# Kernel tuning notes

Hardware: AMD Instinct MI355X
Metric: run time of the kernel (lower is better)

## Reference

```python
import jax, jax.numpy as jnp
import numpy as np

B, C, H, W = 2, 64, 48, 48
NH = 8
EPS = 1e-5


def conv2d(x, w, b=None, pad=0):
    out = jax.lax.conv_general_dilated(x, w, (1, 1), [(pad, pad), (pad, pad)],
                                       dimension_numbers=('NCHW', 'OIHW', 'NCHW'))
    return out if b is None else out + b[None, :, None, None]


def bn2d(x, g, b, m, v):
    # eval-mode BatchNorm2d with running stats
    return (x - m[None, :, None, None]) * (g / jnp.sqrt(v + EPS))[None, :, None, None] + b[None, :, None, None]


def ln(x, g, b):
    mu = x.mean(-1, keepdims=True)
    var = ((x - mu) ** 2).mean(-1, keepdims=True)
    return (x - mu) / jnp.sqrt(var + EPS) * g + b


def _forward(x, y, pconv_w, pconv_b, bnd_g, bnd_b, bnd_m, bnd_v,
             lnx_g, lnx_b, lny_g, lny_b, lnz_g, lnz_b,
             k_w, k_b, qv_w, qv_b, proj_w, proj_b,
             c2w1, c2b1, c2bn1_g, c2bn1_b, c2bn1_m, c2bn1_v,
             c2w2, c2b2, c2bn2_g, c2bn2_b, c2bn2_m, c2bn2_v,
             bn2_g, bn2_b, bn2_m, bn2_v,
             f1w, fbn1_g, fbn1_b, fbn1_m, fbn1_v,
             f2w, fbn2_g, fbn2_b, fbn2_m, fbn2_v,
             f3w, f3b):
    Bq, Cq, Hq, Wq = x.shape
    N = Hq * Wq
    hd = Cq // NH
    scale = hd ** -0.5
    xy = conv2d(jnp.concatenate([x, y], 1), pconv_w, pconv_b, pad=0)
    xb = bn2d(x, bnd_g, bnd_b, bnd_m, bnd_v)
    yb = bn2d(y, bnd_g, bnd_b, bnd_m, bnd_v)
    xyb = bn2d(xy, bnd_g, bnd_b, bnd_m, bnd_v)
    sc1 = xb.reshape(Bq, Cq, N).transpose(0, 2, 1)  # [B,N,C]
    sd1 = yb.reshape(Bq, Cq, N).transpose(0, 2, 1)
    xl = ln(sc1, lnx_g, lnx_b)
    yl = ln(sd1, lny_g, lny_b)
    zl = ln(xyb.reshape(Bq, Cq, N).transpose(0, 2, 1), lnz_g, lnz_b)

    def qv_heads(t):
        qv = (t @ qv_w.T + qv_b).reshape(Bq, N, 2, NH, hd)
        return qv[:, :, 0].transpose(0, 2, 1, 3), qv[:, :, 1].transpose(0, 2, 1, 3)

    x_q, x_v = qv_heads(xl)
    y_q, y_v = qv_heads(yl)
    k = (zl @ k_w.T + k_b).reshape(Bq, N, NH, hd).transpose(0, 2, 1, 3)  # [B,H,N,hd]
    attn1 = jnp.einsum('bhnd,bhmd->bhnm', x_q, k) * scale
    attn2 = jnp.einsum('bhnd,bhmd->bhnm', y_q, k) * scale
    attn = jax.nn.softmax(attn1 * attn2, axis=-1)  # product of two score maps
    xo = jnp.einsum('bhnm,bhmd->bhnd', attn, x_v).transpose(0, 2, 1, 3).reshape(Bq, N, Cq) @ proj_w.T + proj_b
    yo = jnp.einsum('bhnm,bhmd->bhnd', attn, y_v).transpose(0, 2, 1, 3).reshape(Bq, N, Cq) @ proj_w.T + proj_b
    xo = (xo + sc1).transpose(0, 2, 1).reshape(Bq, Cq, Hq, Wq)
    yo = (yo + sd1).transpose(0, 2, 1).reshape(Bq, Cq, Hq, Wq)

    def conv2_block(t):  # shared-weight conv2 applied to both branches
        h = jax.nn.relu(bn2d(conv2d(t, c2w1, c2b1, pad=1), c2bn1_g, c2bn1_b, c2bn1_m, c2bn1_v))
        return jax.nn.relu(bn2d(conv2d(h, c2w2, c2b2, pad=1), c2bn2_g, c2bn2_b, c2bn2_m, c2bn2_v))

    xo = conv2_block(xo) + xo
    yo = conv2_block(yo) + yo
    cat = jnp.concatenate([xo + yo, xo * yo], 1)  # [B,2C,H,W]
    f = bn2d(cat, bn2_g, bn2_b, bn2_m, bn2_v)
    f = jax.nn.relu(bn2d(conv2d(f, f1w, None, pad=1), fbn1_g, fbn1_b, fbn1_m, fbn1_v))
    f = jax.nn.relu(bn2d(conv2d(f, f2w, None, pad=1), fbn2_g, fbn2_b, fbn2_m, fbn2_v))
    f = conv2d(f, f3w, f3b, pad=0)
    return cat + f


def setup_inputs() -> dict:
    ks = iter(jax.random.split(jax.random.key(0), 64))

    def nrm(shape, s=0.05):
        return jax.random.normal(next(ks), shape, jnp.float32) * s

    def bn_params(c):
        return (1.0 + nrm((c,)), nrm((c,)), nrm((c,)),
                jax.random.uniform(next(ks), (c,), jnp.float32, 0.5, 1.5))

    d = {}
    d['x'] = jax.random.normal(next(ks), (B, C, H, W), jnp.float32)
    d['y'] = jax.random.normal(next(ks), (B, C, H, W), jnp.float32)
    d['pconv_w'] = nrm((C, 2 * C, 1, 1)); d['pconv_b'] = nrm((C,))
    d['bnd_g'], d['bnd_b'], d['bnd_m'], d['bnd_v'] = bn_params(C)
    d['lnx_g'] = 1.0 + nrm((C,)); d['lnx_b'] = nrm((C,))
    d['lny_g'] = 1.0 + nrm((C,)); d['lny_b'] = nrm((C,))
    d['lnz_g'] = 1.0 + nrm((C,)); d['lnz_b'] = nrm((C,))
    d['k_w'] = nrm((C, C)); d['k_b'] = nrm((C,))
    d['qv_w'] = nrm((2 * C, C)); d['qv_b'] = nrm((2 * C,))
    d['proj_w'] = nrm((C, C)); d['proj_b'] = nrm((C,))
    d['c2w1'] = nrm((C, C, 3, 3)); d['c2b1'] = nrm((C,))
    d['c2bn1_g'], d['c2bn1_b'], d['c2bn1_m'], d['c2bn1_v'] = bn_params(C)
    d['c2w2'] = nrm((C, C, 3, 3)); d['c2b2'] = nrm((C,))
    d['c2bn2_g'], d['c2bn2_b'], d['c2bn2_m'], d['c2bn2_v'] = bn_params(C)
    d['bn2_g'], d['bn2_b'], d['bn2_m'], d['bn2_v'] = bn_params(2 * C)
    d['f1w'] = nrm((2 * C, 2 * C, 3, 3))
    d['fbn1_g'], d['fbn1_b'], d['fbn1_m'], d['fbn1_v'] = bn_params(2 * C)
    d['f2w'] = nrm((2 * C, 2 * C, 3, 3))
    d['fbn2_g'], d['fbn2_b'], d['fbn2_m'], d['fbn2_v'] = bn_params(2 * C)
    d['f3w'] = nrm((2 * C, 2 * C, 1, 1)); d['f3b'] = nrm((2 * C,))
    return d


def reference(x, y, pconv_w, pconv_b, bnd_g, bnd_b, bnd_m, bnd_v,
              lnx_g, lnx_b, lny_g, lny_b, lnz_g, lnz_b,
              k_w, k_b, qv_w, qv_b, proj_w, proj_b,
              c2w1, c2b1, c2bn1_g, c2bn1_b, c2bn1_m, c2bn1_v,
              c2w2, c2b2, c2bn2_g, c2bn2_b, c2bn2_m, c2bn2_v,
              bn2_g, bn2_b, bn2_m, bn2_v,
              f1w, fbn1_g, fbn1_b, fbn1_m, fbn1_v,
              f2w, fbn2_g, fbn2_b, fbn2_m, fbn2_v,
              f3w, f3b):
    return _forward(x, y, pconv_w, pconv_b, bnd_g, bnd_b, bnd_m, bnd_v,
                    lnx_g, lnx_b, lny_g, lny_b, lnz_g, lnz_b,
                    k_w, k_b, qv_w, qv_b, proj_w, proj_b,
                    c2w1, c2b1, c2bn1_g, c2bn1_b, c2bn1_m, c2bn1_v,
                    c2w2, c2b2, c2bn2_g, c2bn2_b, c2bn2_m, c2bn2_v,
                    bn2_g, bn2_b, bn2_m, bn2_v,
                    f1w, fbn1_g, fbn1_b, fbn1_m, fbn1_v,
                    f2w, fbn2_g, fbn2_b, fbn2_m, fbn2_v,
                    f3w, f3b)
```

## Files before the change

kernel.cpp:

```cpp
#include <hip/hip_runtime.h>
#include <hip/hip_bf16.h>

#define B_   2
#define C_   64
#define H_   48
#define W_   48
#define N_   (H_*W_)
#define NH_  8
#define HD_  8
#define EPS_ 1e-5f
#define S2_  0.125f
#define LOG2E_ 1.44269504f
#define FS_  (S2_ * LOG2E_)
#define S_   ((size_t)B_ * C_ * N_)
#define CN_  ((size_t)C_ * N_)
#define XTSZ_ ((size_t)(N_ + 2 * W_) * 128)
#define XTSC_ ((size_t)(N_ + 2 * W_) * 64)

typedef unsigned short u16;
typedef __attribute__((ext_vector_type(8))) short short8v;
typedef __attribute__((ext_vector_type(4))) float f32x4;
union F8 { uint4 u4; short8v s; unsigned int w[4]; };

__device__ __forceinline__ float wsum64(float v) {
#pragma unroll
  for (int o = 32; o > 0; o >>= 1) v += __shfl_xor(v, o, 64);
  return v;
}

__device__ __forceinline__ float ln_val(float t, float g, float b) {
  float mu  = wsum64(t) * (1.0f / 64.0f);
  float d   = t - mu;
  float var = wsum64(d * d) * (1.0f / 64.0f);
  return d * rsqrtf(var + EPS_) * g + b;
}

__device__ __forceinline__ u16 f2bf(float x) {
  union { float f; unsigned int u; } a; a.f = x;
  unsigned int r = a.u + 0x7fffu + ((a.u >> 16) & 1u);
  return (u16)(r >> 16);
}

__global__ __launch_bounds__(1024) void k_pre(
    const float* __restrict__ x, const float* __restrict__ y,
    const float* __restrict__ pw, const float* __restrict__ pb,
    const float* g, const float* bb, const float* m, const float* v,
    const float* lnxg, const float* lnxb,
    const float* lnyg, const float* lnyb,
    const float* lnzg, const float* lnzb,
    float* __restrict__ xl, float* __restrict__ yl, float* __restrict__ zl) {
  __shared__ float4 pwT[32][64];
  __shared__ float xs[16][64], ys[16][64];
  int w = threadIdx.x >> 6, c = threadIdx.x & 63;
  for (int idx = threadIdx.x; idx < 2048; idx += 1024) {
    int cc = idx & 63, i4 = idx >> 6;
    pwT[i4][cc] = *(const float4*)(pw + (size_t)cc * 2 * C_ + i4 * 4);
  }
  int row = blockIdx.x * 16 + w;
  int b = row / N_, n = row % N_;
  float xv = x[(size_t)(b * C_ + c) * N_ + n];
  float yv = y[(size_t)(b * C_ + c) * N_ + n];
  xs[w][c] = xv; ys[w][c] = yv;
  __syncthreads();
  const float4* xw = (const float4*)xs[w];
  const float4* yw = (const float4*)ys[w];
  float acc = pb[c];
#pragma unroll
  for (int t = 0; t < 16; ++t) {
    float4 a = xw[t], wv = pwT[t][c];
    acc += a.x * wv.x + a.y * wv.y + a.z * wv.z + a.w * wv.w;
  }
#pragma unroll
  for (int t = 0; t < 16; ++t) {
    float4 a = yw[t], wv = pwT[16 + t][c];
    acc += a.x * wv.x + a.y * wv.y + a.z * wv.z + a.w * wv.w;
  }
  float s  = g[c] * rsqrtf(v[c] + EPS_);
  float sh = bb[c] - m[c] * s;
  float tx = xv * s + sh;
  xl[(size_t)row * C_ + c] = ln_val(tx, lnxg[c], lnxb[c]);
  float ty = yv * s + sh;
  yl[(size_t)row * C_ + c] = ln_val(ty, lnyg[c], lnyb[c]);
  float tz = acc * s + sh;
  zl[(size_t)row * C_ + c] = ln_val(tz, lnzg[c], lnzb[c]);
}

__global__ __launch_bounds__(64) void k_qvk(
    const float* __restrict__ xl, const float* __restrict__ yl,
    const float* __restrict__ zl,
    const float* __restrict__ qvw, const float* __restrict__ qvb,
    const float* __restrict__ kw, const float* __restrict__ kb,
    u16* __restrict__ qxb, u16* __restrict__ qyb,
    u16* __restrict__ kbf, u16* __restrict__ vt) {
  int l = threadIdx.x;
  int part = blockIdx.y >> 2;
  int j0 = (blockIdx.y & 3) * 16;
  int row = blockIdx.x * 64 + l;
  int b = row / N_, n = row % N_;
  const float* inp = (part < 2) ? xl : (part < 4) ? yl : zl;
  float4 in[16];
  const float4* ir = (const float4*)(inp + (size_t)row * C_);
#pragma unroll
  for (int t = 0; t < 16; ++t) in[t] = ir[t];

  const float* wb   = (part == 4) ? kw : qvw;
  const float* bias = (part == 4) ? kb : qvb;
  int joff = (part == 1 || part == 3) ? 64 : 0;

  if (part == 1 || part == 3) {
    int vbase = (part == 1) ? 0 : 8;
#pragma unroll
    for (int jj = 0; jj < 16; ++jj) {
      int j = j0 + jj;
      const float4* wr = (const float4*)(wb + (size_t)(joff + j) * C_);
      float acc = bias[joff + j];
#pragma unroll
      for (int t = 0; t < 16; ++t) {
        float4 a = in[t], wv = wr[t];
        acc += a.x * wv.x + a.y * wv.y + a.z * wv.z + a.w * wv.w;
      }
      int h = j >> 3, d = j & 7;
      vt[((size_t)((b * NH_ + h) * 16 + vbase + d)) * N_ + n] = f2bf(acc);
    }
  } else {
    u16* dst = (part == 0) ? qxb : (part == 2) ? qyb : kbf;
#pragma unroll
    for (int gg = 0; gg < 2; ++gg) {
      int h = (j0 >> 3) + gg;
      union { uint4 u4; u16 s[8]; } pk;
#pragma unroll
      for (int d = 0; d < 8; ++d) {
        int j = h * 8 + d;
        const float4* wr = (const float4*)(wb + (size_t)(joff + j) * C_);
        float acc = bias[joff + j];
#pragma unroll
        for (int t = 0; t < 16; ++t) {
          float4 a = in[t], wv = wr[t];
          acc += a.x * wv.x + a.y * wv.y + a.z * wv.z + a.w * wv.w;
        }
        if (part == 0) acc *= FS_;
        pk.s[d] = f2bf(acc);
      }
      *(uint4*)(dst + ((size_t)(b * NH_ + h) * N_ + n) * 8) = pk.u4;
    }
  }
}

__global__ __launch_bounds__(128, 5) void k_attn8(
    const u16* __restrict__ qx, const u16* __restrict__ qy,
    const u16* __restrict__ kk, const u16* __restrict__ vt,
    float* __restrict__ outx, float* __restrict__ outy) {
  __shared__ float sAcc[2][4][64];
  __shared__ float sL[2][16];
  int qt = blockIdx.x, bh = blockIdx.y;
  int tid = threadIdx.x;
  int lane = tid & 63;
  int wave = tid >> 6;
  int l15 = lane & 15;
  int q0 = qt * 16;

  F8 qxf, qyf;
  size_t qoff = ((size_t)bh * N_ + q0 + l15) * 8;
  qxf.u4 = *(const uint4*)(qx + qoff);
  qyf.u4 = *(const uint4*)(qy + qoff);
  if (lane >= 16) {
    qxf.u4 = make_uint4(0u, 0u, 0u, 0u);
    qyf.u4 = make_uint4(0u, 0u, 0u, 0u);
  }

  int key0 = wave * (N_ / 2);
  const uint4* kp = (const uint4*)(kk + (size_t)bh * N_ * 8) + key0 + l15;
  const uint4* vp = (const uint4*)(vt + ((size_t)bh * 16 + l15) * N_ + key0)
                    + (lane >> 4);
  int addr0 = (((lane >> 4) & 1) * 32 + l15) * 4;
  int addr1 = addr0 + 64;
  int thi = lane >> 5;

  f32x4 acc = {0.f, 0.f, 0.f, 0.f};
  const f32x4 z4 = {0.f, 0.f, 0.f, 0.f};
  float lsum = 0.f;

  F8 ka, kb2, vf;
  ka.u4 = kp[0]; kb2.u4 = kp[16]; vf.u4 = *vp;
  for (int c = 0; c < 36; ++c) {
    F8 kaC = ka, kbC = kb2, vfC = vf;
    kp += 32; vp += 4;
    ka.u4 = kp[0]; kb2.u4 = kp[16]; vf.u4 = *vp;

    f32x4 s1a = __builtin_amdgcn_mfma_f32_16x16x32_bf16(kaC.s, qxf.s, z4, 0, 0, 0);
    f32x4 s2a = __builtin_amdgcn_mfma_f32_16x16x32_bf16(kaC.s, qyf.s, z4, 0, 0, 0);
    f32x4 s1b = __builtin_amdgcn_mfma_f32_16x16x32_bf16(kbC.s, qxf.s, z4, 0, 0, 0);
    f32x4 s2b = __builtin_amdgcn_mfma_f32_16x16x32_bf16(kbC.s, qyf.s, z4, 0, 0, 0);

    float p00 = exp2f(s1a[0] * s2a[0]), p01 = exp2f(s1a[1] * s2a[1]);
    float p02 = exp2f(s1a[2] * s2a[2]), p03 = exp2f(s1a[3] * s2a[3]);
    float p10 = exp2f(s1b[0] * s2b[0]), p11 = exp2f(s1b[1] * s2b[1]);
    float p12 = exp2f(s1b[2] * s2b[2]), p13 = exp2f(s1b[3] * s2b[3]);
    lsum += ((p00 + p01) + (p02 + p03)) + ((p10 + p11) + (p12 + p13));

    unsigned int pk00, pk10, pk01, pk11;
    asm("v_cvt_pk_bf16_f32 %0, %1, %2" : "=v"(pk00) : "v"(p00), "v"(p01));
    asm("v_cvt_pk_bf16_f32 %0, %1, %2" : "=v"(pk10) : "v"(p02), "v"(p03));
    asm("v_cvt_pk_bf16_f32 %0, %1, %2" : "=v"(pk01) : "v"(p10), "v"(p11));
    asm("v_cvt_pk_bf16_f32 %0, %1, %2" : "=v"(pk11) : "v"(p12), "v"(p13));

    int b00 = __builtin_amdgcn_ds_bpermute(addr0, (int)pk00);
    int b01 = __builtin_amdgcn_ds_bpermute(addr0, (int)pk01);
    int b10 = __builtin_amdgcn_ds_bpermute(addr0, (int)pk10);
    int b11 = __builtin_amdgcn_ds_bpermute(addr0, (int)pk11);
    int c00 = __builtin_amdgcn_ds_bpermute(addr1, (int)pk00);
    int c01 = __builtin_amdgcn_ds_bpermute(addr1, (int)pk01);
    int c10 = __builtin_amdgcn_ds_bpermute(addr1, (int)pk10);
    int c11 = __builtin_amdgcn_ds_bpermute(addr1, (int)pk11);

    F8 pf;
    pf.w[0] = (unsigned int)(thi ? b01 : b00);
    pf.w[1] = (unsigned int)(thi ? b11 : b10);
    pf.w[2] = (unsigned int)(thi ? c01 : c00);
    pf.w[3] = (unsigned int)(thi ? c11 : c10);
    acc = __builtin_amdgcn_mfma_f32_16x16x32_bf16(pf.s, vfC.s, acc, 0, 0, 0);
  }

  lsum += __shfl_xor(lsum, 16, 64);
  lsum += __shfl_xor(lsum, 32, 64);
  if (lane < 16) sL[wave][lane] = lsum;
#pragma unroll
  for (int r = 0; r < 4; ++r) sAcc[wave][r][lane] = acc[r];
  __syncthreads();
  if (wave == 0) {
    float Linv = 1.f / (sL[0][l15] + sL[1][l15]);
    int b = bh >> 3, h = bh & 7;
    int d = l15 & 7;
    float* ob = (l15 < 8) ? outx : outy;
    size_t cbase = (size_t)b * N_ * C_ + (size_t)h * 8 + d;
#pragma unroll
    for (int r = 0; r < 4; ++r) {
      int qrow = 4 * (lane >> 4) + r;
      float li = __shfl(Linv, qrow, 64);
      float a = sAcc[0][r][lane] + sAcc[1][r][lane];
      ob[cbase + (size_t)(q0 + qrow) * C_] = a * li;
    }
  }
}

__global__ __launch_bounds__(64) void k_proj4(
    const float* __restrict__ attbase,
    const float* __restrict__ x, const float* __restrict__ y,
    const float* bg, const float* bb2, const float* bm, const float* bv,
    const float* __restrict__ pw, const float* __restrict__ pbias,
    float* __restrict__ outbase, u16* __restrict__ xt0) {
  __shared__ float attT[64][66];
  int tid = threadIdx.x;
  int p0 = blockIdx.x * 64;
  int c0 = blockIdx.y * 2;
  int z = blockIdx.z;
  int branch = z >> 1, b = z & 1;
  const float* att = attbase + branch * S_ + (size_t)b * N_ * C_;
  for (int r = 0; r < 64; ++r)
    attT[tid][r] = att[(size_t)(p0 + r) * C_ + tid];
  __syncthreads();
  int p = p0 + tid;
  const float* w0 = pw + (size_t)c0 * C_;
  const float* w1 = w0 + C_;
  float a0 = pbias[c0], a1 = pbias[c0 + 1];
#pragma unroll 8
  for (int c = 0; c < C_; ++c) {
    float av = attT[c][tid];
    a0 += av * w0[c];
    a1 += av * w1[c];
  }
  float s0  = bg[c0] * rsqrtf(bv[c0] + EPS_);
  float sh0 = bb2[c0] - bm[c0] * s0;
  float s1  = bg[c0+1] * rsqrtf(bv[c0+1] + EPS_);
  float sh1 = bb2[c0+1] - bm[c0+1] * s1;
  const float* xin = branch ? y : x;
  float r0 = xin[((size_t)b * C_ + c0) * N_ + p];
  float r1 = xin[((size_t)b * C_ + c0 + 1) * N_ + p];
  float v0 = a0 + r0 * s0 + sh0;
  float v1 = a1 + r1 * s1 + sh1;
  size_t o = (size_t)z * CN_ + (size_t)c0 * N_ + p;
  outbase[o]      = v0;
  outbase[o + N_] = v1;
  unsigned int pv = ((unsigned int)f2bf(v1) << 16) | (unsigned int)f2bf(v0);
  *(unsigned int*)(xt0 + (size_t)z * XTSC_ + (size_t)(W_ + p) * 64 + c0) = pv;
}

__global__ void k_catbn(const float* __restrict__ o2,
                        const float* __restrict__ g, const float* __restrict__ b2,
                        const float* __restrict__ m, const float* __restrict__ v,
                        float* __restrict__ cat, u16* __restrict__ xt1) {
  int t = blockIdx.x * 256 + threadIdx.x;
  int p4 = t * 4;
  int n  = p4 % N_;
  int c2 = (p4 / N_) % (2 * C_);
  int b  = p4 / (2 * C_ * N_);
  int c  = c2 & 63;
  float4 X = *(const float4*)(o2 + (size_t)b * CN_ + (size_t)c * N_ + n);
  float4 Y = *(const float4*)(o2 + (size_t)(2 + b) * CN_ + (size_t)c * N_ + n);
  float4 val;
  if (c2 < C_) val = make_float4(X.x + Y.x, X.y + Y.y, X.z + Y.z, X.w + Y.w);
  else         val = make_float4(X.x * Y.x, X.y * Y.y, X.z * Y.z, X.w * Y.w);
  size_t co = ((size_t)b * 2 * C_ + c2) * N_ + n;
  *(float4*)(cat + co) = val;
  float s  = g[c2] * rsqrtf(v[c2] + EPS_);
  float sh = b2[c2] - m[c2] * s;
  u16* xb = xt1 + (size_t)b * XTSZ_ + (size_t)(W_ + n) * 128 + c2;
  xb[0]   = f2bf(val.x * s + sh);
  xb[128] = f2bf(val.y * s + sh);
  xb[256] = f2bf(val.z * s + sh);
  xb[384] = f2bf(val.w * s + sh);
}

__global__ void k_zg(u16* __restrict__ b0, u16* __restrict__ b1,
                     int nimg, int cinc) {
  int gsz = W_ * cinc / 2;
  int pbt = nimg * 2 * gsz;
  int idx = blockIdx.x * 256 + threadIdx.x;
  if (idx >= 2 * pbt) return;
  u16* base = (idx < pbt) ? b0 : b1;
  int r = idx % pbt;
  int img = r / (2 * gsz);
  int r2 = r % (2 * gsz);
  int hi = r2 / gsz, o = r2 % gsz;
  size_t xts = (size_t)(N_ + 2 * W_) * cinc;
  ((unsigned int*)(base + (size_t)img * xts
                   + (hi ? (size_t)(W_ + N_) * cinc : 0)))[o] = 0u;
}

__global__ void k_wcvt(const float* __restrict__ w1,
                       const float* __restrict__ w2,
                       const float* __restrict__ cw1,
                       const float* __restrict__ cw2,
                       u16* __restrict__ wb) {
  int idx = blockIdx.x * 256 + threadIdx.x;
  if (idx >= 368640) return;
  if (idx < 294912) {
    int layer = idx / 147456, rem = idx - layer * 147456;
    int t = rem / 16384, r2 = rem - t * 16384;
    int co = r2 >> 7, ci = r2 & 127;
    wb[idx] = f2bf((layer ? w2 : w1)[(size_t)co * 1152 + ci * 9 + t]);
  } else {
    int k = idx - 294912;
    int layer = k / 36864, rem = k - layer * 36864;
    int t = rem / 4096, r2 = rem - t * 4096;
    int co = r2 >> 6, ci = r2 & 63;
    wb[idx] = f2bf((layer ? cw2 : cw1)[(size_t)co * 576 + ci * 9 + t]);
  }
}

template<int MODE>
__global__ __launch_bounds__(64) void k_fmma(
    const u16* __restrict__ xt, const u16* __restrict__ wb,
    const float* __restrict__ cbias,
    const float* g, const float* b2, const float* m, const float* v,
    const float* __restrict__ resid,
    u16* __restrict__ xto, float* __restrict__ fo) {
  constexpr int CIN  = (MODE >= 2) ? 64 : 128;
  constexpr int NCB  = CIN / 32;
  constexpr int COUT = (MODE >= 2) ? 64 : 128;
  constexpr int TS   = CIN * COUT;
  constexpr size_t XTS = (size_t)(N_ + 2 * W_) * CIN;
  constexpr size_t XTSO = (size_t)(N_ + 2 * W_) * COUT;
  int l = threadIdx.x;
  int c = l & 15, gg = l >> 4;
  int px0 = blockIdx.x * 16;
  int ct0 = blockIdx.y * 16;
  int b = blockIdx.z;
  int x0 = px0 % W_;
  bool mL = (x0 == 0) && (c == 0);
  bool mR = (x0 == 32) && (c == 15);
  const u16* xb = xt + (size_t)b * XTS + (size_t)W_ * CIN;
  const u16* aw = wb + (size_t)(ct0 + c) * CIN + gg * 8;

  f32x4 acc = {0.f, 0.f, 0.f, 0.f};
#pragma unroll
  for (int cb = 0; cb < NCB; ++cb) {
#pragma unroll
    for (int t = 0; t < 9; ++t) {
      const int dx = t % 3 - 1, dy = t / 3 - 1;
      F8 af, bf;
      af.u4 = *(const uint4*)(aw + t * TS + cb * 32);
      int px = px0 + c + dx + dy * W_;
      px = max(px, -W_);
      bf.u4 = *(const uint4*)(xb + (ptrdiff_t)px * CIN + cb * 32 + gg * 8);
      bool msk = (dx < 0 && mL) || (dx > 0 && mR);
      if (msk) bf.u4 = make_uint4(0u, 0u, 0u, 0u);
      acc = __builtin_amdgcn_mfma_f32_16x16x32_bf16(af.s, bf.s, acc, 0, 0, 0);
    }
  }
  int px = px0 + c;
  if (MODE == 0 || MODE == 2) {
    union { ushort4 u; u16 s[4]; } pk;
#pragma unroll
    for (int r = 0; r < 4; ++r) {
      int cout = ct0 + 4 * gg + r;
      float a = acc[r] + (MODE == 2 ? cbias[cout] : 0.f);
      float s = g[cout] * rsqrtf(v[cout] + EPS_);
      float sh = b2[cout] - m[cout] * s;
      pk.s[r] = f2bf(fmaxf(a * s + sh, 0.f));
    }
    *(ushort4*)(xto + (size_t)b * XTSO + (size_t)(W_ + px) * COUT
                + ct0 + 4 * gg) = pk.u;
  } else if (MODE == 1) {
#pragma unroll
    for (int r = 0; r < 4; ++r) {
      int cout = ct0 + 4 * gg + r;
      fo[(size_t)b * S_ + (size_t)cout * N_ + px] = acc[r];
    }
  } else {
#pragma unroll
    for (int r = 0; r < 4; ++r) {
      int cout = ct0 + 4 * gg + r;
      float a = acc[r] + cbias[cout];
      float s = g[cout] * rsqrtf(v[cout] + EPS_);
      float sh = b2[cout] - m[cout] * s;
      size_t off = (size_t)b * CN_ + (size_t)cout * N_ + px;
      fo[off] = fmaxf(a * s + sh, 0.f) + resid[off];
    }
  }
}

__global__ __launch_bounds__(64) void k_final3(
    const float* __restrict__ ff, size_t strideF,
    const float* __restrict__ g2, const float* __restrict__ b2,
    const float* __restrict__ m2, const float* __restrict__ v2,
    const float* __restrict__ cat,
    const float* __restrict__ w, const float* __restrict__ fb,
    float* __restrict__ out) {
  __shared__ float fsc[2 * C_], fsh[2 * C_];
  for (int j = threadIdx.x; j < 2 * C_; j += 64) {
    float s = g2[j] * rsqrtf(v2[j] + EPS_);
    fsc[j] = s;
    fsh[j] = b2[j] - m2[j] * s;
  }
  __syncthreads();
  int p = blockIdx.x * 128 + threadIdx.x * 2;
  int c0 = blockIdx.y * 2;
  int b = blockIdx.z;
  const float* fr = ff + (size_t)b * strideF;
  const float* wr0 = w + (size_t)c0 * 2 * C_;
  const float* wr1 = wr0 + 2 * C_;
  float a00 = fb[c0], a01 = a00;
  float a10 = fb[c0 + 1], a11 = a10;
#pragma unroll 4
  for (int j = 0; j < 2 * C_; ++j) {
    float2 fa = *(const float2*)(fr + (size_t)j * N_ + p);
    float s = fsc[j], sh = fsh[j];
    float f0 = fmaxf(fa.x * s + sh, 0.f);
    float f1 = fmaxf(fa.y * s + sh, 0.f);
    float wv0 = wr0[j], wv1 = wr1[j];
    a00 += wv0 * f0; a01 += wv0 * f1;
    a10 += wv1 * f0; a11 += wv1 * f1;
  }
  size_t o = ((size_t)b * 2 * C_ + c0) * N_ + p;
  float2 cv0 = *(const float2*)(cat + o);
  float2 cv1 = *(const float2*)(cat + o + N_);
  *(float2*)(out + o)      = make_float2(a00 + cv0.x, a01 + cv0.y);
  *(float2*)(out + o + N_) = make_float2(a10 + cv1.x, a11 + cv1.y);
}

extern "C" void kernel_launch(void* const* d_in, const int* in_sizes, int n_in,
                              void* d_out, int out_size, void* d_ws, size_t ws_size,
                              hipStream_t stream) {
  const float* x       = (const float*)d_in[0];
  const float* y       = (const float*)d_in[1];
  const float* pconv_w = (const float*)d_in[2];
  const float* pconv_b = (const float*)d_in[3];
  const float* bnd_g = (const float*)d_in[4];
  const float* bnd_b = (const float*)d_in[5];
  const float* bnd_m = (const float*)d_in[6];
  const float* bnd_v = (const float*)d_in[7];
  const float* lnx_g = (const float*)d_in[8];
  const float* lnx_b = (const float*)d_in[9];
  const float* lny_g = (const float*)d_in[10];
  const float* lny_b = (const float*)d_in[11];
  const float* lnz_g = (const float*)d_in[12];
  const float* lnz_b = (const float*)d_in[13];
  const float* k_w   = (const float*)d_in[14];
  const float* k_b   = (const float*)d_in[15];
  const float* qv_w  = (const float*)d_in[16];
  const float* qv_b  = (const float*)d_in[17];
  const float* proj_w = (const float*)d_in[18];
  const float* proj_b = (const float*)d_in[19];
  const float* c2w1  = (const float*)d_in[20];
  const float* c2b1  = (const float*)d_in[21];
  const float* c2bn1_g = (const float*)d_in[22];
  const float* c2bn1_b = (const float*)d_in[23];
  const float* c2bn1_m = (const float*)d_in[24];
  const float* c2bn1_v = (const float*)d_in[25];
  const float* c2w2  = (const float*)d_in[26];
  const float* c2b2  = (const float*)d_in[27];
  const float* c2bn2_g = (const float*)d_in[28];
  const float* c2bn2_b = (const float*)d_in[29];
  const float* c2bn2_m = (const float*)d_in[30];
  const float* c2bn2_v = (const float*)d_in[31];
  const float* bn2_g = (const float*)d_in[32];
  const float* bn2_b = (const float*)d_in[33];
  const float* bn2_m = (const float*)d_in[34];
  const float* bn2_v = (const float*)d_in[35];
  const float* f1w   = (const float*)d_in[36];
  const float* fbn1_g = (const float*)d_in[37];
  const float* fbn1_b = (const float*)d_in[38];
  const float* fbn1_m = (const float*)d_in[39];
  const float* fbn1_v = (const float*)d_in[40];
  const float* f2w   = (const float*)d_in[41];
  const float* fbn2_g = (const float*)d_in[42];
  const float* fbn2_b = (const float*)d_in[43];
  const float* fbn2_m = (const float*)d_in[44];
  const float* fbn2_v = (const float*)d_in[45];
  const float* f3w   = (const float*)d_in[46];
  const float* f3b   = (const float*)d_in[47];

  float* ws = (float*)d_ws;
  float* sl1 = ws + 1 * S_;
  float* sl2 = ws + 2 * S_;
  float* sl3 = ws + 3 * S_;
  float* sl5 = ws + 5 * S_;
  u16* xtC0 = (u16*)sl5;
  u16* xtC1 = (u16*)ws;
  u16* xtF1 = (u16*)(ws + 3 * S_ / 2);
  u16* xtF2 = (u16*)ws;
  float* xo4 = sl3;
  float* o2  = sl5;
  float* f2o = sl5;
  u16* wb   = (u16*)(ws + 7 * S_);
  u16* wbf1 = wb;
  u16* wbf2 = wb + 147456;
  u16* wbc1 = wb + 294912;
  u16* wbc2 = wb + 331776;

  k_pre<<<B_ * N_ / 16, 1024, 0, stream>>>(x, y, pconv_w, pconv_b,
                                    bnd_g, bnd_b, bnd_m, bnd_v,
                                    lnx_g, lnx_b, lny_g, lny_b, lnz_g, lnz_b,
                                    sl1, sl2, sl3);
  k_wcvt<<<1440, 256, 0, stream>>>(f1w, f2w, c2w1, c2w2, wb);
  u16* qxb = (u16*)(ws + 4 * S_);
  u16* qyb = qxb + (size_t)B_ * NH_ * N_ * 8;
  u16* kbf = (u16*)sl5;
  u16* vtb = (u16*)(ws + 6 * S_);
  {
    dim3 g(B_ * N_ / 64, 20);
    k_qvk<<<g, 64, 0, stream>>>(sl1, sl2, sl3, qv_w, qv_b, k_w, k_b,
                                qxb, qyb, kbf, vtb);
  }
  {
    dim3 g(N_ / 16, B_ * NH_);
    k_attn8<<<g, 128, 0, stream>>>(qxb, qyb, kbf, vtb, sl1, sl2);
  }
  {
    dim3 g(36, C_ / 2, 2 * B_);
    k_proj4<<<g, 64, 0, stream>>>(sl1, x, y, bnd_g, bnd_b, bnd_m, bnd_v,
                                  proj_w, proj_b, xo4, xtC0);
  }
  k_zg<<<96, 256, 0, stream>>>(xtC0, xtC1, 4, 64);
  {
    dim3 g(N_ / 16, 4, 4);
    k_fmma<2><<<g, 64, 0, stream>>>(xtC0, wbc1, c2b1,
        c2bn1_g, c2bn1_b, c2bn1_m, c2bn1_v, nullptr, xtC1, nullptr);
  }
  {
    dim3 g(N_ / 16, 4, 4);
    k_fmma<3><<<g, 64, 0, stream>>>(xtC1, wbc2, c2b2,
        c2bn2_g, c2bn2_b, c2bn2_m, c2bn2_v, xo4, nullptr, o2);
  }
  k_zg<<<96, 256, 0, stream>>>(xtF1, xtF2, 2, 128);
  k_catbn<<<576, 256, 0, stream>>>(o2, bn2_g, bn2_b, bn2_m, bn2_v,
                                   sl3, xtF1);
  {
    dim3 g(N_ / 16, 8, B_);
    k_fmma<0><<<g, 64, 0, stream>>>(xtF1, wbf1, nullptr,
        fbn1_g, fbn1_b, fbn1_m, fbn1_v, nullptr, xtF2, nullptr);
    k_fmma<1><<<g, 64, 0, stream>>>(xtF2, wbf2, nullptr,
        nullptr, nullptr, nullptr, nullptr, nullptr, nullptr, f2o);
  }
  {
    dim3 g(18, C_, B_);
    k_final3<<<g, 64, 0, stream>>>(f2o, S_,
                                   fbn2_g, fbn2_b, fbn2_m, fbn2_v,
                                   sl3, f3w, f3b, (float*)d_out);
  }
}
```

Measured before the change: 321.8 us.

## Move projection and final 1x1 conv to bf16 MFMA with bf16 intermediates

The attention output is now stored as bf16, and the output projection is redone as a 16x16x32 bf16 MFMA kernel using projection weights pre-converted in the weight-conversion kernel. The second FFN 3x3 conv now applies BN+ReLU in its epilogue and writes a padded bf16 tensor, which a new MFMA-based 1x1 conv kernel consumes in place of the scalar fp32 final kernel. Halo zeroing is merged into one launch plus the catbn kernel, and workspace buffers are reassigned. This cuts scalar FP32 FMA work and memory traffic at the cost of extra bf16 rounding on the attention output and the FFN activations.

After: 304.9 us. 1.06x faster.

```diff
diff --git a/kernel.cpp b/kernel.cpp
--- a/kernel.cpp
+++ b/kernel.cpp
@@ -149,7 +149,7 @@
 __global__ __launch_bounds__(128, 5) void k_attn8(
     const u16* __restrict__ qx, const u16* __restrict__ qy,
     const u16* __restrict__ kk, const u16* __restrict__ vt,
-    float* __restrict__ outx, float* __restrict__ outy) {
+    u16* __restrict__ outx, u16* __restrict__ outy) {
   __shared__ float sAcc[2][4][64];
   __shared__ float sL[2][16];
   int qt = blockIdx.x, bh = blockIdx.y;
@@ -231,65 +231,66 @@
     float Linv = 1.f / (sL[0][l15] + sL[1][l15]);
     int b = bh >> 3, h = bh & 7;
     int d = l15 & 7;
-    float* ob = (l15 < 8) ? outx : outy;
+    u16* ob = (l15 < 8) ? outx : outy;
     size_t cbase = (size_t)b * N_ * C_ + (size_t)h * 8 + d;
 #pragma unroll
     for (int r = 0; r < 4; ++r) {
       int qrow = 4 * (lane >> 4) + r;
       float li = __shfl(Linv, qrow, 64);
       float a = sAcc[0][r][lane] + sAcc[1][r][lane];
-      ob[cbase + (size_t)(q0 + qrow) * C_] = a * li;
+      ob[cbase + (size_t)(q0 + qrow) * C_] = f2bf(a * li);
     }
   }
 }
 
-__global__ __launch_bounds__(64) void k_proj4(
-    const float* __restrict__ attbase,
+__global__ __launch_bounds__(64) void k_projm(
+    const u16* __restrict__ attx, const u16* __restrict__ atty,
     const float* __restrict__ x, const float* __restrict__ y,
     const float* bg, const float* bb2, const float* bm, const float* bv,
-    const float* __restrict__ pw, const float* __restrict__ pbias,
-    float* __restrict__ outbase, u16* __restrict__ xt0) {
-  __shared__ float attT[64][66];
-  int tid = threadIdx.x;
-  int p0 = blockIdx.x * 64;
-  int c0 = blockIdx.y * 2;
+    const u16* __restrict__ pwb, const float* __restrict__ pbias,
+    float* __restrict__ xo4, u16* __restrict__ xt0) {
+  int l = threadIdx.x;
+  int c = l & 15, gg = l >> 4;
+  int px0 = blockIdx.x * 16;
+  int ct0 = blockIdx.y * 16;
   int z = blockIdx.z;
   int branch = z >> 1, b = z & 1;
-  const float* att = attbase + branch * S_ + (size_t)b * N_ * C_;
-  for (int r = 0; r < 64; ++r)
-    attT[tid][r] = att[(size_t)(p0 + r) * C_ + tid];
-  __syncthreads();
-  int p = p0 + tid;
-  const float* w0 = pw + (size_t)c0 * C_;
-  const float* w1 = w0 + C_;
-  float a0 = pbias[c0], a1 = pbias[c0 + 1];
-#pragma unroll 8
-  for (int c = 0; c < C_; ++c) {
-    float av = attT[c][tid];
-    a0 += av * w0[c];
-    a1 += av * w1[c];
-  }
-  float s0  = bg[c0] * rsqrtf(bv[c0] + EPS_);
-  float sh0 = bb2[c0] - bm[c0] * s0;
-  float s1  = bg[c0+1] * rsqrtf(bv[c0+1] + EPS_);
-  float sh1 = bb2[c0+1] - bm[c0+1] * s1;
+  const u16* att = (branch ? atty : attx) + (size_t)b * N_ * 64;
+  const u16* aw = pwb + (size_t)(ct0 + c) * 64 + gg * 8;
+  f32x4 acc = {0.f, 0.f, 0.f, 0.f};
+#pragma unroll
+  for (int cb = 0; cb < 2; ++cb) {
+    F8 af, bf;
+    af.u4 = *(const uint4*)(aw + cb * 32);
+    bf.u4 = *(const uint4*)(att + (size_t)(px0 + c) * 64 + cb * 32 + gg * 8);
+    acc = __builtin_amdgcn_mfma_f32_16x16x32_bf16(af.s, bf.s, acc, 0, 0, 0);
+  }
+  int px = px0 + c;
   const float* xin = branch ? y : x;
-  float r0 = xin[((size_t)b * C_ + c0) * N_ + p];
-  float r1 = xin[((size_t)b * C_ + c0 + 1) * N_ + p];
-  float v0 = a0 + r0 * s0 + sh0;
-  float v1 = a1 + r1 * s1 + sh1;
-  size_t o = (size_t)z * CN_ + (size_t)c0 * N_ + p;
-  outbase[o]      = v0;
-  outbase[o + N_] = v1;
-  unsigned int pv = ((unsigned int)f2bf(v1) << 16) | (unsigned int)f2bf(v0);
-  *(unsigned int*)(xt0 + (size_t)z * XTSC_ + (size_t)(W_ + p) * 64 + c0) = pv;
+#pragma unroll
+  for (int r = 0; r < 4; ++r) {
+    int cout = ct0 + 4 * gg + r;
+    float s  = bg[cout] * rsqrtf(bv[cout] + EPS_);
+    float sh = bb2[cout] - bm[cout] * s;
+    float rr = xin[((size_t)b * C_ + cout) * N_ + px];
+    float vv = acc[r] + pbias[cout] + rr * s + sh;
+    xo4[(size_t)z * CN_ + (size_t)cout * N_ + px] = vv;
+    xt0[(size_t)z * XTSC_ + (size_t)(W_ + px) * 64 + cout] = f2bf(vv);
+  }
 }
 
 __global__ void k_catbn(const float* __restrict__ o2,
                         const float* __restrict__ g, const float* __restrict__ b2,
                         const float* __restrict__ m, const float* __restrict__ v,
-                        float* __restrict__ cat, u16* __restrict__ xt1) {
+                        float* __restrict__ cat, u16* __restrict__ xt1,
+                        u16* __restrict__ xtf2) {
   int t = blockIdx.x * 256 + threadIdx.x;
+  if (t < 12288) {
+    int img = t / 6144, r2 = t - img * 6144;
+    int hi = r2 / 3072, o = r2 - hi * 3072;
+    ((unsigned int*)(xtf2 + (size_t)img * XTSZ_
+                     + (hi ? (size_t)(W_ + N_) * 128 : 0)))[o] = 0u;
+  }
   int p4 = t * 4;
   int n  = p4 % N_;
   int c2 = (p4 / N_) % (2 * C_);
@@ -311,19 +312,19 @@
   xb[384] = f2bf(val.w * s + sh);
 }
 
-__global__ void k_zg(u16* __restrict__ b0, u16* __restrict__ b1,
-                     int nimg, int cinc) {
+__global__ void k_zg1(u16* __restrict__ c0, u16* __restrict__ c1,
+                      u16* __restrict__ f1) {
+  int idx = blockIdx.x * 256 + threadIdx.x;
+  if (idx >= 36864) return;
+  int seg = idx / 12288, r = idx - seg * 12288;
+  u16* base; int cinc;
+  if (seg == 0)      { base = c0; cinc = 64; }
+  else if (seg == 1) { base = c1; cinc = 64; }
+  else               { base = f1; cinc = 128; }
   int gsz = W_ * cinc / 2;
-  int pbt = nimg * 2 * gsz;
-  int idx = blockIdx.x * 256 + threadIdx.x;
-  if (idx >= 2 * pbt) return;
-  u16* base = (idx < pbt) ? b0 : b1;
-  int r = idx % pbt;
-  int img = r / (2 * gsz);
-  int r2 = r % (2 * gsz);
-  int hi = r2 / gsz, o = r2 % gsz;
-  size_t xts = (size_t)(N_ + 2 * W_) * cinc;
-  ((unsigned int*)(base + (size_t)img * xts
+  int img = r / (2 * gsz), r2 = r - img * (2 * gsz);
+  int hi = r2 / gsz, o = r2 - hi * gsz;
+  ((unsigned int*)(base + (size_t)img * (N_ + 2 * W_) * cinc
                    + (hi ? (size_t)(W_ + N_) * cinc : 0)))[o] = 0u;
 }
 
@@ -331,20 +332,26 @@
                        const float* __restrict__ w2,
                        const float* __restrict__ cw1,
                        const float* __restrict__ cw2,
+                       const float* __restrict__ w3,
+                       const float* __restrict__ pjw,
                        u16* __restrict__ wb) {
   int idx = blockIdx.x * 256 + threadIdx.x;
-  if (idx >= 368640) return;
+  if (idx >= 389120) return;
   if (idx < 294912) {
     int layer = idx / 147456, rem = idx - layer * 147456;
     int t = rem / 16384, r2 = rem - t * 16384;
     int co = r2 >> 7, ci = r2 & 127;
     wb[idx] = f2bf((layer ? w2 : w1)[(size_t)co * 1152 + ci * 9 + t]);
-  } else {
+  } else if (idx < 368640) {
     int k = idx - 294912;
     int layer = k / 36864, rem = k - layer * 36864;
     int t = rem / 4096, r2 = rem - t * 4096;
     int co = r2 >> 6, ci = r2 & 63;
     wb[idx] = f2bf((layer ? cw2 : cw1)[(size_t)co * 576 + ci * 9 + t]);
+  } else if (idx < 385024) {
+    wb[idx] = f2bf(w3[idx - 368640]);
+  } else {
+    wb[idx] = f2bf(pjw[idx - 385024]);
   }
 }
 
@@ -401,12 +408,6 @@
     }
     *(ushort4*)(xto + (size_t)b * XTSO + (size_t)(W_ + px) * COUT
                 + ct0 + 4 * gg) = pk.u;
-  } else if (MODE == 1) {
-#pragma unroll
-    for (int r = 0; r < 4; ++r) {
-      int cout = ct0 + 4 * gg + r;
-      fo[(size_t)b * S_ + (size_t)cout * N_ + px] = acc[r];
-    }
   } else {
 #pragma unroll
     for (int r = 0; r < 4; ++r) {
@@ -420,43 +421,32 @@
   }
 }
 
-__global__ __launch_bounds__(64) void k_final3(
-    const float* __restrict__ ff, size_t strideF,
-    const float* __restrict__ g2, const float* __restrict__ b2,
-    const float* __restrict__ m2, const float* __restrict__ v2,
-    const float* __restrict__ cat,
-    const float* __restrict__ w, const float* __restrict__ fb,
+__global__ __launch_bounds__(64) void k_f3mma(
+    const u16* __restrict__ xt3, const u16* __restrict__ w3b,
+    const float* __restrict__ f3b, const float* __restrict__ cat,
     float* __restrict__ out) {
-  __shared__ float fsc[2 * C_], fsh[2 * C_];
-  for (int j = threadIdx.x; j < 2 * C_; j += 64) {
-    float s = g2[j] * rsqrtf(v2[j] + EPS_);
-    fsc[j] = s;
-    fsh[j] = b2[j] - m2[j] * s;
-  }
-  __syncthreads();
-  int p = blockIdx.x * 128 + threadIdx.x * 2;
-  int c0 = blockIdx.y * 2;
+  int l = threadIdx.x;
+  int c = l & 15, gg = l >> 4;
+  int px0 = blockIdx.x * 16;
+  int ct0 = blockIdx.y * 16;
   int b = blockIdx.z;
-  const float* fr = ff + (size_t)b * strideF;
-  const float* wr0 = w + (size_t)c0 * 2 * C_;
-  const float* wr1 = wr0 + 2 * C_;
-  float a00 = fb[c0], a01 = a00;
-  float a10 = fb[c0 + 1], a11 = a10;
-#pragma unroll 4
-  for (int j = 0; j < 2 * C_; ++j) {
-    float2 fa = *(const float2*)(fr + (size_t)j * N_ + p);
-    float s = fsc[j], sh = fsh[j];
-    float f0 = fmaxf(fa.x * s + sh, 0.f);
-    float f1 = fmaxf(fa.y * s + sh, 0.f);
-    float wv0 = wr0[j], wv1 = wr1[j];
-    a00 += wv0 * f0; a01 += wv0 * f1;
-    a10 += wv1 * f0; a11 += wv1 * f1;
-  }
-  size_t o = ((size_t)b * 2 * C_ + c0) * N_ + p;
-  float2 cv0 = *(const float2*)(cat + o);
-  float2 cv1 = *(const float2*)(cat + o + N_);
-  *(float2*)(out + o)      = make_float2(a00 + cv0.x, a01 + cv0.y);
-  *(float2*)(out + o + N_) = make_float2(a10 + cv1.x, a11 + cv1.y);
+  const u16* xb = xt3 + (size_t)b * XTSZ_ + (size_t)W_ * 128;
+  const u16* aw = w3b + (size_t)(ct0 + c) * 128 + gg * 8;
+  f32x4 acc = {0.f, 0.f, 0.f, 0.f};
+#pragma unroll
+  for (int cb = 0; cb < 4; ++cb) {
+    F8 af, bf;
+    af.u4 = *(const uint4*)(aw + cb * 32);
+    bf.u4 = *(const uint4*)(xb + (size_t)(px0 + c) * 128 + cb * 32 + gg * 8);
+    acc = __builtin_amdgcn_mfma_f32_16x16x32_bf16(af.s, bf.s, acc, 0, 0, 0);
+  }
+  int px = px0 + c;
+#pragma unroll
+  for (int r = 0; r < 4; ++r) {
+    int cout = ct0 + 4 * gg + r;
+    size_t off = ((size_t)b * 2 * C_ + cout) * N_ + px;
+    out[off] = acc[r] + f3b[cout] + cat[off];
+  }
 }
 
 extern "C" void kernel_launch(void* const* d_in, const int* in_sizes, int n_in,
@@ -515,28 +505,32 @@
   float* sl1 = ws + 1 * S_;
   float* sl2 = ws + 2 * S_;
   float* sl3 = ws + 3 * S_;
-  float* sl5 = ws + 5 * S_;
-  u16* xtC0 = (u16*)sl5;
+  u16* attx = (u16*)(ws + 1 * S_);
+  u16* atty = attx + (size_t)B_ * N_ * 64;
+  u16* xtC0 = (u16*)(ws + 5 * S_);
   u16* xtC1 = (u16*)ws;
-  u16* xtF1 = (u16*)(ws + 3 * S_ / 2);
+  u16* xtF1 = (u16*)(ws + 5 * S_ / 4);
   u16* xtF2 = (u16*)ws;
-  float* xo4 = sl3;
-  float* o2  = sl5;
-  float* f2o = sl5;
+  u16* xt3  = (u16*)(ws + 5 * S_ / 4);
+  float* xo4 = ws + 3 * S_;
+  float* o2  = ws + 5 * S_;
+  float* cat = ws + 3 * S_;
   u16* wb   = (u16*)(ws + 7 * S_);
   u16* wbf1 = wb;
   u16* wbf2 = wb + 147456;
   u16* wbc1 = wb + 294912;
   u16* wbc2 = wb + 331776;
+  u16* wb3  = wb + 368640;
+  u16* wbp  = wb + 385024;
 
   k_pre<<<B_ * N_ / 16, 1024, 0, stream>>>(x, y, pconv_w, pconv_b,
                                     bnd_g, bnd_b, bnd_m, bnd_v,
                                     lnx_g, lnx_b, lny_g, lny_b, lnz_g, lnz_b,
                                     sl1, sl2, sl3);
-  k_wcvt<<<1440, 256, 0, stream>>>(f1w, f2w, c2w1, c2w2, wb);
+  k_wcvt<<<1520, 256, 0, stream>>>(f1w, f2w, c2w1, c2w2, f3w, proj_w, wb);
   u16* qxb = (u16*)(ws + 4 * S_);
   u16* qyb = qxb + (size_t)B_ * NH_ * N_ * 8;
-  u16* kbf = (u16*)sl5;
+  u16* kbf = (u16*)(ws + 5 * S_);
   u16* vtb = (u16*)(ws + 6 * S_);
   {
     dim3 g(B_ * N_ / 64, 20);
@@ -545,14 +539,15 @@
   }
   {
     dim3 g(N_ / 16, B_ * NH_);
-    k_attn8<<<g, 128, 0, stream>>>(qxb, qyb, kbf, vtb, sl1, sl2);
-  }
-  {
-    dim3 g(36, C_ / 2, 2 * B_);
-    k_proj4<<<g, 64, 0, stream>>>(sl1, x, y, bnd_g, bnd_b, bnd_m, bnd_v,
-                                  proj_w, proj_b, xo4, xtC0);
-  }
-  k_zg<<<96, 256, 0, stream>>>(xtC0, xtC1, 4, 64);
+    k_attn8<<<g, 128, 0, stream>>>(qxb, qyb, kbf, vtb, attx, atty);
+  }
+  {
+    dim3 g(N_ / 16, 4, 4);
+    k_projm<<<g, 64, 0, stream>>>(attx, atty, x, y,
+                                  bnd_g, bnd_b, bnd_m, bnd_v,
+                                  wbp, proj_b, xo4, xtC0);
+  }
+  k_zg1<<<144, 256, 0, stream>>>(xtC0, xtC1, xtF1);
   {
     dim3 g(N_ / 16, 4, 4);
     k_fmma<2><<<g, 64, 0, stream>>>(xtC0, wbc1, c2b1,
@@ -563,20 +558,17 @@
     k_fmma<3><<<g, 64, 0, stream>>>(xtC1, wbc2, c2b2,
         c2bn2_g, c2bn2_b, c2bn2_m, c2bn2_v, xo4, nullptr, o2);
   }
-  k_zg<<<96, 256, 0, stream>>>(xtF1, xtF2, 2, 128);
   k_catbn<<<576, 256, 0, stream>>>(o2, bn2_g, bn2_b, bn2_m, bn2_v,
-                                   sl3, xtF1);
+                                   cat, xtF1, xtF2);
   {
     dim3 g(N_ / 16, 8, B_);
     k_fmma<0><<<g, 64, 0, stream>>>(xtF1, wbf1, nullptr,
         fbn1_g, fbn1_b, fbn1_m, fbn1_v, nullptr, xtF2, nullptr);
-    k_fmma<1><<<g, 64, 0, stream>>>(xtF2, wbf2, nullptr,
-        nullptr, nullptr, nullptr, nullptr, nullptr, nullptr, f2o);
-  }
-  {
-    dim3 g(18, C_, B_);
-    k_final3<<<g, 64, 0, stream>>>(f2o, S_,
-                                   fbn2_g, fbn2_b, fbn2_m, fbn2_v,
-                                   sl3, f3w, f3b, (float*)d_out);
-  }
-}
+    k_fmma<0><<<g, 64, 0, stream>>>(xtF2, wbf2, nullptr,
+        fbn2_g, fbn2_b, fbn2_m, fbn2_v, nullptr, xt3, nullptr);
+  }
+  {
+    dim3 g(N_ / 16, 8, B_);
+    k_f3mma<<<g, 64, 0, stream>>>(xt3, wb3, f3b, cat, (float*)d_out);
+  }
+}
```
